# Performance work log

Hardware: AMD Instinct MI355X
Metric: run time of the kernel (lower is better)

Reference implementation:

```python
import jax, jax.numpy as jnp
import numpy as np
from jax import lax

BITWIDTH = 7
EPS = 1e-5


def ti_quant(x):
    """TiFloatToInt8: per-tensor int8 quantization with power-of-2 scale."""
    rng = jnp.max(jnp.abs(x))
    bw = jnp.ceil(jnp.log2(rng))
    exp = bw - BITWIDTH
    q = jnp.clip(jnp.round(x * 2.0 ** (BITWIDTH - bw)), -128.0, 127.0)
    return q, exp


def ti_conv(xv, xe, wv, we, pad):
    """TiConv2d: integer conv (simulated in f32, all values int-valued),
    int32 accumulate, then shift back to 8 bits; exponents add."""
    acc = lax.conv_general_dilated(
        xv, wv, window_strides=(1, 1), padding=[(pad, pad), (pad, pad)],
        dimension_numbers=("NCHW", "OIHW", "NCHW"))
    rng = jnp.max(jnp.abs(acc))
    bw = jnp.ceil(jnp.log2(rng))
    shift = jnp.maximum(bw - BITWIDTH, 0.0)
    q = jnp.clip(jnp.round(acc * 2.0 ** (-shift)), -128.0, 127.0)
    return q, xe + we + shift


def batchnorm(x, gamma, beta):
    # training-mode BN: batch statistics over (N, H, W)
    mean = jnp.mean(x, axis=(0, 2, 3), keepdims=True)
    var = jnp.var(x, axis=(0, 2, 3), keepdims=True)
    g = gamma[None, :, None, None]
    b = beta[None, :, None, None]
    return g * (x - mean) * lax.rsqrt(var + EPS) + b


def setup_inputs() -> dict:
    key = jax.random.key(0)
    k0, k1, k2, k3, k4 = jax.random.split(key, 5)
    B, Cin, Cout, H, W = 32, 128, 256, 56, 56
    x_val = jax.random.randint(k0, (B, Cin, H, W), -128, 128, dtype=jnp.int32)
    x_exp = jnp.zeros((), jnp.float32) - 7.0
    wDW = jnp.round(jnp.clip(jax.random.normal(k1, (Cin, Cin, 3, 3), jnp.float32) * 32.0, -128.0, 127.0))
    wDW_exp = jnp.zeros((), jnp.float32) - 9.0
    wPW = jnp.round(jnp.clip(jax.random.normal(k2, (Cout, Cin, 1, 1), jnp.float32) * 32.0, -128.0, 127.0))
    wPW_exp = jnp.zeros((), jnp.float32) - 9.0
    gamma1 = jnp.ones((Cin,), jnp.float32) + 0.1 * jax.random.normal(k3, (Cin,), jnp.float32)
    beta1 = jnp.zeros((Cin,), jnp.float32)
    gamma2 = jnp.ones((Cout,), jnp.float32) + 0.1 * jax.random.normal(k4, (Cout,), jnp.float32)
    beta2 = jnp.zeros((Cout,), jnp.float32)
    return {"x_val": x_val, "x_exp": x_exp, "wDW": wDW, "wDW_exp": wDW_exp,
            "wPW": wPW, "wPW_exp": wPW_exp, "gamma1": gamma1, "beta1": beta1,
            "gamma2": gamma2, "beta2": beta2}


def reference(x_val, x_exp, wDW, wDW_exp, wPW, wPW_exp, gamma1, beta1, gamma2, beta2):
    xv = x_val.astype(jnp.float32)
    # convDW (3x3, in->in, pad=1)
    q, e = ti_conv(xv, x_exp, wDW, wDW_exp, 1)
    # dequant -> bn1 -> quant
    f = batchnorm(q * 2.0 ** e, gamma1, beta1)
    q, e = ti_quant(f)
    # TiReLU on int values
    q = jnp.maximum(q, 0.0)
    # convPW (1x1, in->out)
    q, e = ti_conv(q, e, wPW, wPW_exp, 0)
    # dequant -> bn2 -> quant -> relu
    f = batchnorm(q * 2.0 ** e, gamma2, beta2)
    q, e = ti_quant(f)
    q = jnp.maximum(q, 0.0)
    return q.astype(jnp.int8), e
```

## Files before the change

### kernel.cpp

```cpp
#include <hip/hip_runtime.h>
#include <cstdint>
#include <cstddef>

#define C1 128
#define C2 256
#define Hh 56
#define Wd 56
#define HW 3136
#define NHW 100352
#define N1 ((size_t)12845056)
#define N2 ((size_t)25690112)
#define XPSZ ((size_t)13778944)
#define NREP 8
#define NB1 392
#define NB2C 392

typedef int v4i __attribute__((ext_vector_type(4)));
typedef int v16i __attribute__((ext_vector_type(16)));

static constexpr size_t OFF_XP = 0;
static constexpr size_t OFF_Q1 = XPSZ;
static constexpr size_t OFF_Q3 = OFF_Q1 + N1;
static constexpr size_t OFF_WQ1 = OFF_Q3 + N2;
static constexpr size_t OFF_WQ2 = OFF_WQ1 + 147456;
static constexpr size_t OFF_STATS = OFF_WQ2 + 32768;

struct Stats {
  int absmax1, absmax2, pad0, pad1;
  float scale1, e1, s2, e2;
  float scaleq2, e3, sf, ef;
  int padA[20];
  int tick1, padB[31];
  int tick2, padC[31];
  int tick3, padD[31];
  int tick4, padE[31];
  int sum1[NREP][C1]; unsigned sumsq1[NREP][C1];
  int min1[NREP][C1], max1[NREP][C1];
  float A1[C1], B1c[C1];
  int sum2[NREP][C2]; unsigned sumsq2[NREP][C2];
  int min2[NREP][C2], max2[NREP][C2];
  float A2[C2], B2c[C2];
};

__global__ __launch_bounds__(256) void k_pre(
    const int* __restrict__ x, signed char* __restrict__ xp,
    const float* __restrict__ wDW, signed char* __restrict__ wq1t,
    const float* __restrict__ wPW, signed char* __restrict__ wq2t,
    Stats* st) {
  __shared__ signed char lds[56 * 132];
  int t = threadIdx.x, bid = blockIdx.x;
  if (bid < 1856) {
    int hh = bid % 58, n = bid / 58;
    int* xpw = (int*)(xp + ((size_t)n * 58 + hh) * 7424);
    if (hh == 0 || hh == 57) {
      for (int o = t; o < 1856; o += 256) xpw[o] = 0;
      return;
    }
    int h = hh - 1;
    const int4* xb4 = (const int4*)(x + (size_t)n * C1 * HW + h * 56);
    for (int idx = t; idx < 1792; idx += 256) {
      int c = idx / 14, wq = idx - c * 14;
      int4 v = xb4[(size_t)c * 784 + wq];
      int w = wq * 4;
      lds[(w + 0) * 132 + c] = (signed char)v.x;
      lds[(w + 1) * 132 + c] = (signed char)v.y;
      lds[(w + 2) * 132 + c] = (signed char)v.z;
      lds[(w + 3) * 132 + c] = (signed char)v.w;
    }
    __syncthreads();
    for (int o = t; o < 1856; o += 256) {
      int kb = o / 232, r = o - kb * 232, ww = r >> 2, cw = r & 3;
      int val = (ww == 0 || ww == 57) ? 0
                : *(const int*)&lds[(ww - 1) * 132 + kb * 16 + cw * 4];
      xpw[o] = val;
    }
    return;
  }
  if (bid < 2432) {
    int idx = (bid - 1856) * 256 + t;
    int co = idx / 1152, r = idx - co * 1152;
    int ci = r / 9, pos = r - ci * 9;
    int k = pos * 128 + ci;
    wq1t[(size_t)(k >> 4) * 2048 + co * 16 + (k & 15)] = (signed char)(int)wDW[idx];
    return;
  }
  if (bid < 2560) {
    int i = (bid - 2432) * 256 + t;
    int co = i >> 7, ci = i & 127;
    wq2t[(size_t)(ci >> 4) * 4096 + co * 16 + (ci & 15)] = (signed char)(int)wPW[i];
    return;
  }
  if (t == 0) {
    st->absmax1 = 0; st->absmax2 = 0;
    st->tick1 = 0; st->tick2 = 0; st->tick3 = 0; st->tick4 = 0;
  }
  for (int c = t; c < NREP * C1; c += 256) {
    ((int*)st->sum1)[c] = 0; ((unsigned*)st->sumsq1)[c] = 0u;
    ((int*)st->min1)[c] = 127; ((int*)st->max1)[c] = -128;
  }
  for (int c = t; c < NREP * C2; c += 256) {
    ((int*)st->sum2)[c] = 0; ((unsigned*)st->sumsq2)[c] = 0u;
    ((int*)st->min2)[c] = 127; ((int*)st->max2)[c] = -128;
  }
}

__device__ inline v4i ld16_lds(const signed char* p) {
  const int2* q = (const int2*)p;
  int2 lo = q[0], hi = q[1];
  v4i r; r[0] = lo.x; r[1] = lo.y; r[2] = hi.x; r[3] = hi.y;
  return r;
}

__device__ inline float bn_affine_v(int sum, unsigned sumsq, int mn, int mx,
                                    float g, float b, float e_in,
                                    float* Aout, float* Bout) {
  double meanq = (double)sum / (double)NHW;
  double varq = (double)sumsq / (double)NHW - meanq * meanq;
  float se = exp2f(e_in);
  float mean = (float)meanq * se;
  float var = (float)varq * se * se;
  float rsq = 1.0f / sqrtf(var + 1e-5f);
  float Avv = g * se * rsq;
  float Bvv = b - g * mean * rsq;
  *Aout = Avv; *Bout = Bvv;
  return fmaxf(fabsf(Avv * (float)mn + Bvv), fabsf(Avv * (float)mx + Bvv));
}

__device__ inline void conv1_mfma(const signed char* __restrict__ xp,
                                  const signed char* __restrict__ wq1t,
                                  int bx, int t, v16i a1[2][4]) {
  int lane = t & 63, wave = t >> 6;
  int half = lane >> 5, l31 = lane & 31;
  size_t g0 = (size_t)bx * 256;

  const signed char* ab[2];
#pragma unroll
  for (int i = 0; i < 2; ++i) {
    size_t gm = g0 + wave * 64 + i * 32 + l31;
    int n = (int)(gm / HW);
    int p = (int)(gm - (size_t)n * HW);
    int h = p / 56, w = p - h * 56;
    ab[i] = xp + ((size_t)n * 58 + h) * 7424 + w * 16 + half * 928;
  }
  const signed char* bb[4];
#pragma unroll
  for (int j = 0; j < 4; ++j)
    bb[j] = wq1t + (size_t)(j * 32 + l31) * 16 + half * 2048;

#pragma unroll
  for (int i = 0; i < 2; ++i)
#pragma unroll
    for (int j = 0; j < 4; ++j)
#pragma unroll
      for (int r = 0; r < 16; ++r) a1[i][j][r] = 0;

#pragma unroll
  for (int pos = 0; pos < 9; ++pos) {
    int kh = pos / 3, kw = pos - kh * 3;
    const signed char* a0p = ab[0] + kh * 7424 + kw * 16;
    const signed char* a1p = ab[1] + kh * 7424 + kw * 16;
#pragma unroll
    for (int kb = 0; kb < 8; kb += 2) {
      v4i af0 = *(const v4i*)(a0p + kb * 928);
      v4i af1 = *(const v4i*)(a1p + kb * 928);
      v4i bf[4];
#pragma unroll
      for (int j = 0; j < 4; ++j)
        bf[j] = *(const v4i*)(bb[j] + pos * 16384 + kb * 2048);
#pragma unroll
      for (int j = 0; j < 4; ++j) {
        a1[0][j] = __builtin_amdgcn_mfma_i32_32x32x32_i8(af0, bf[j], a1[0][j], 0, 0, 0);
        a1[1][j] = __builtin_amdgcn_mfma_i32_32x32x32_i8(af1, bf[j], a1[1][j], 0, 0, 0);
      }
    }
  }
}

__global__ __launch_bounds__(256, 2) void k_conv1f(
    const signed char* __restrict__ xp, const signed char* __restrict__ wq1t,
    signed char* __restrict__ q1, Stats* st,
    const float* __restrict__ x_exp, const float* __restrict__ wDW_exp,
    const float* __restrict__ gamma1, const float* __restrict__ beta1) {
  __shared__ int reda[4];
  __shared__ int vbro;
  __shared__ int qti[256 * 34];
  __shared__ int psum[C1], psq[C1], pmn[C1], pmx[C1];
  __shared__ float redc[2];
  __shared__ int lastf;
  signed char* qt = (signed char*)qti;
  int t = threadIdx.x, lane = t & 63, wave = t >> 6;
  int half = lane >> 5, l31 = lane & 31;
  int rep = blockIdx.x & (NREP - 1);

  v16i a1[2][4];
  conv1_mfma(xp, wq1t, blockIdx.x, t, a1);

  int am = 0;
#pragma unroll
  for (int i = 0; i < 2; ++i)
#pragma unroll
    for (int j = 0; j < 4; ++j)
#pragma unroll
      for (int r = 0; r < 16; ++r) am = max(am, abs(a1[i][j][r]));
  for (int off = 32; off; off >>= 1) am = max(am, __shfl_down(am, off, 64));
  if (lane == 0) reda[wave] = am;
  if (t < C1) { psum[t] = 0; psq[t] = 0; pmn[t] = 127; pmx[t] = -128; }
  __syncthreads();
  if (t == 0)
    atomicMax(&st->absmax1, max(max(reda[0], reda[1]), max(reda[2], reda[3])));
  __syncthreads();

  if (t == 0) {
    atomicAdd(&st->tick1, 1);
    while (atomicAdd(&st->tick1, 0) < NB1)
      __builtin_amdgcn_s_sleep(8);
    vbro = atomicAdd(&st->absmax1, 0);
  }
  __syncthreads();

  int v1 = vbro;
  int pw = 31 - __clz(v1 | 1);
  int bw = ((v1 & (v1 - 1)) == 0) ? pw : pw + 1;
  int sh = max(bw - 7, 0);
  float scale1 = exp2f((float)(-sh));
  float e1 = x_exp[0] + wDW_exp[0] + (float)sh;
  if (blockIdx.x == 0 && t == 0) st->e1 = e1;

#pragma unroll
  for (int j = 0; j < 4; ++j) {
    int sj = 0, sqj = 0, mnj = 127, mxj = -128;
    int c = j * 32 + l31;
#pragma unroll
    for (int i = 0; i < 2; ++i)
#pragma unroll
      for (int reg = 0; reg < 16; ++reg) {
        int av = a1[i][j][reg];
        int row = (reg & 3) + 8 * (reg >> 2) + 4 * half;
        int pix = wave * 64 + i * 32 + row;
        float r = rintf((float)av * scale1);
        r = fminf(fmaxf(r, -128.f), 127.f);
        int qi = (int)r;
        qt[pix * 136 + c] = (signed char)qi;
        sj += qi; sqj += qi * qi; mnj = min(mnj, qi); mxj = max(mxj, qi);
      }
    sj += __shfl_down(sj, 32, 64);
    sqj += __shfl_down(sqj, 32, 64);
    mnj = min(mnj, __shfl_down(mnj, 32, 64));
    mxj = max(mxj, __shfl_down(mxj, 32, 64));
    if (half == 0) {
      atomicAdd(&psum[c], sj); atomicAdd(&psq[c], sqj);
      atomicMin(&pmn[c], mnj); atomicMax(&pmx[c], mxj);
    }
  }
  __syncthreads();
  if (t < C1) {
    atomicAdd(&st->sum1[rep][t], psum[t]);
    atomicAdd(&st->sumsq1[rep][t], (unsigned)psq[t]);
    atomicMin(&st->min1[rep][t], pmn[t]);
    atomicMax(&st->max1[rep][t], pmx[t]);
  }
  int* q1w = (int*)(q1 + (size_t)blockIdx.x * 256 * 128);
  for (int idx = t; idx < 8192; idx += 256)
    q1w[idx] = qti[(idx >> 5) * 34 + (idx & 31)];

  __syncthreads();
  if (t == 0) lastf = (atomicAdd(&st->tick3, 1) == NB1 - 1);
  __syncthreads();
  if (lastf) {
    if (t < C1) {
      int sm = 0; unsigned sq = 0; int mn = 127, mx = -128;
#pragma unroll
      for (int r2 = 0; r2 < NREP; ++r2) {
        sm += atomicAdd(&st->sum1[r2][t], 0);
        sq += atomicAdd(&st->sumsq1[r2][t], 0u);
        mn = min(mn, atomicMin(&st->min1[r2][t], 127));
        mx = max(mx, atomicMax(&st->max1[r2][t], -128));
      }
      float cand = bn_affine_v(sm, sq, mn, mx, gamma1[t], beta1[t], e1,
                               &st->A1[t], &st->B1c[t]);
      for (int off = 32; off; off >>= 1) cand = fmaxf(cand, __shfl_down(cand, off, 64));
      if ((t & 63) == 0) redc[t >> 6] = cand;
    }
    __syncthreads();
    if (t == 0) {
      float rng = fmaxf(redc[0], redc[1]);
      float bwv = ceilf(log2f(rng));
      st->s2 = exp2f(7.0f - bwv);
      st->e2 = bwv - 7.0f;
    }
  }
}

__global__ __launch_bounds__(256, 2) void k_conv2f(
    const signed char* __restrict__ q1, const signed char* __restrict__ wq2t,
    signed char* __restrict__ q3, Stats* st, const float* __restrict__ wPW_exp,
    const float* __restrict__ gamma2, const float* __restrict__ beta2,
    float* __restrict__ out) {
  __shared__ int qti[256 * 34];
  __shared__ int psum[C2], psq[C2], pmn[C2], pmx[C2];
  __shared__ int reda[4];
  __shared__ float red2[4];
  __shared__ int vbro, lastf;
  signed char* qt = (signed char*)qti;

  int t = threadIdx.x, lane = t & 63, wave = t >> 6;
  int half = lane >> 5, l31 = lane & 31;
  size_t g0 = (size_t)blockIdx.x * 256;
  int rep = blockIdx.x & (NREP - 1);

  psum[t] = 0; psq[t] = 0; pmn[t] = 127; pmx[t] = -128;

  int c4 = t & 31;
  float Av[4], Bv[4];
#pragma unroll
  for (int jj = 0; jj < 4; ++jj) {
    Av[jj] = st->A1[c4 * 4 + jj];
    Bv[jj] = st->B1c[c4 * 4 + jj];
  }
  float s2 = st->s2;
  const int* q1w = (const int*)(q1 + g0 * 128);
#pragma unroll
  for (int k = 0; k < 32; ++k) {
    int idx = k * 256 + t;
    int v = q1w[idx];
    int pix = idx >> 5;
    int outv = 0;
#pragma unroll
    for (int jj = 0; jj < 4; ++jj) {
      int b = (signed char)(v >> (8 * jj));
      float y = Av[jj] * (float)b + Bv[jj];
      float r = rintf(y * s2);
      r = fminf(fmaxf(r, -128.f), 127.f);
      r = fmaxf(r, 0.f);
      outv |= ((int)r & 0xff) << (8 * jj);
    }
    qti[pix * 34 + c4] = outv;
  }
  __syncthreads();

  int am2 = 0;
#pragma unroll
  for (int pg = 0; pg < 2; ++pg) {
    int prow = pg * 128 + wave * 32 + l31;
#pragma unroll
    for (int h2 = 0; h2 < 2; ++h2) {
      v16i acc[4];
#pragma unroll
      for (int j = 0; j < 4; ++j)
#pragma unroll
        for (int r = 0; r < 16; ++r) acc[j][r] = 0;
#pragma unroll
      for (int ks = 0; ks < 4; ++ks) {
        v4i af = ld16_lds(&qt[prow * 136 + half * 16 + ks * 32]);
#pragma unroll
        for (int j = 0; j < 4; ++j) {
          v4i bf = *(const v4i*)(wq2t + (size_t)(ks * 2 + half) * 4096 +
                                 ((h2 * 4 + j) * 32 + l31) * 16);
          acc[j] = __builtin_amdgcn_mfma_i32_32x32x32_i8(af, bf, acc[j], 0, 0, 0);
        }
      }
#pragma unroll
      for (int j = 0; j < 4; ++j)
#pragma unroll
        for (int r = 0; r < 16; ++r) am2 = max(am2, abs(acc[j][r]));
    }
  }
  for (int off = 32; off; off >>= 1) am2 = max(am2, __shfl_down(am2, off, 64));
  if (lane == 0) reda[wave] = am2;
  __syncthreads();
  if (t == 0)
    atomicMax(&st->absmax2, max(max(reda[0], reda[1]), max(reda[2], reda[3])));
  __syncthreads();

  if (t == 0) {
    atomicAdd(&st->tick4, 1);
    while (atomicAdd(&st->tick4, 0) < NB2C)
      __builtin_amdgcn_s_sleep(8);
    vbro = atomicAdd(&st->absmax2, 0);
  }
  __syncthreads();

  int v2 = vbro;
  int pw = 31 - __clz(v2 | 1);
  int bw = ((v2 & (v2 - 1)) == 0) ? pw : pw + 1;
  int sh2 = max(bw - 7, 0);
  float scale2 = exp2f((float)(-sh2));
  float e3 = st->e2 + wPW_exp[0] + (float)sh2;
  if (blockIdx.x == 0 && t == 0) st->e3 = e3;

#pragma unroll
  for (int pg = 0; pg < 2; ++pg) {
    int prow = pg * 128 + wave * 32 + l31;
    int* q3w = (int*)(q3 + (size_t)blockIdx.x * 65536 + pg * 32768);
#pragma unroll
    for (int h2 = 0; h2 < 2; ++h2) {
      v16i acc[4];
#pragma unroll
      for (int j = 0; j < 4; ++j)
#pragma unroll
        for (int r = 0; r < 16; ++r) acc[j][r] = 0;
#pragma unroll
      for (int ks = 0; ks < 4; ++ks) {
        v4i af = ld16_lds(&qt[prow * 136 + half * 16 + ks * 32]);
#pragma unroll
        for (int j = 0; j < 4; ++j) {
          v4i bf = *(const v4i*)(wq2t + (size_t)(ks * 2 + half) * 4096 +
                                 ((h2 * 4 + j) * 32 + l31) * 16);
          acc[j] = __builtin_amdgcn_mfma_i32_32x32x32_i8(af, bf, acc[j], 0, 0, 0);
        }
      }
#pragma unroll
      for (int j = 0; j < 4; ++j) {
        int jg = h2 * 4 + j;
        int c = jg * 32 + l31;
        int sj = 0, sqj = 0, mnj = 127, mxj = -128;
#pragma unroll
        for (int rg = 0; rg < 4; ++rg) {
          int pk = 0;
#pragma unroll
          for (int b = 0; b < 4; ++b) {
            float r = rintf((float)acc[j][4 * rg + b] * scale2);
            r = fminf(fmaxf(r, -128.f), 127.f);
            int qi = (int)r;
            pk |= (qi & 0xff) << (8 * b);
            sj += qi; sqj += qi * qi; mnj = min(mnj, qi); mxj = max(mxj, qi);
          }
          q3w[((wave * 8 + jg) * 4 + rg) * 64 + lane] = pk;
        }
        sj += __shfl_down(sj, 32, 64);
        sqj += __shfl_down(sqj, 32, 64);
        mnj = min(mnj, __shfl_down(mnj, 32, 64));
        mxj = max(mxj, __shfl_down(mxj, 32, 64));
        if (half == 0) {
          atomicAdd(&psum[c], sj); atomicAdd(&psq[c], sqj);
          atomicMin(&pmn[c], mnj); atomicMax(&pmx[c], mxj);
        }
      }
    }
  }
  __syncthreads();
  atomicAdd(&st->sum2[rep][t], psum[t]);
  atomicAdd(&st->sumsq2[rep][t], (unsigned)psq[t]);
  atomicMin(&st->min2[rep][t], pmn[t]);
  atomicMax(&st->max2[rep][t], pmx[t]);

  __syncthreads();
  if (t == 0) lastf = (atomicAdd(&st->tick2, 1) == NB2C - 1);
  __syncthreads();
  if (lastf) {
    int sm = 0; unsigned sq = 0; int mn = 127, mx = -128;
#pragma unroll
    for (int r2 = 0; r2 < NREP; ++r2) {
      sm += atomicAdd(&st->sum2[r2][t], 0);
      sq += atomicAdd(&st->sumsq2[r2][t], 0u);
      mn = min(mn, atomicMin(&st->min2[r2][t], 127));
      mx = max(mx, atomicMax(&st->max2[r2][t], -128));
    }
    float cand = bn_affine_v(sm, sq, mn, mx, gamma2[t], beta2[t], e3,
                             &st->A2[t], &st->B2c[t]);
    for (int off = 32; off; off >>= 1) cand = fmaxf(cand, __shfl_down(cand, off, 64));
    if (lane == 0) red2[wave] = cand;
    __syncthreads();
    if (t == 0) {
      float rng = fmaxf(fmaxf(red2[0], red2[1]), fmaxf(red2[2], red2[3]));
      float bwv = ceilf(log2f(rng));
      st->sf = exp2f(7.0f - bwv);
      st->ef = bwv - 7.0f;
      out[N2] = bwv - 7.0f;
    }
  }
}

__global__ __launch_bounds__(256) void k_out(
    const signed char* __restrict__ q3, const Stats* __restrict__ st,
    float* __restrict__ out) {
  __shared__ int ldsc[256 * 17];
  int t = threadIdx.x, lane = t & 63, wave = t >> 6;
  int bid = blockIdx.x;
  size_t g0 = (size_t)bid * 64;
  int n = (int)(g0 / HW), p0 = (int)(g0 - (size_t)n * HW);
  const int* q3r = (const int*)(q3 + (size_t)(bid >> 1) * 32768) + (bid & 1) * 4096;
#pragma unroll
  for (int k = 0; k < 16; ++k) {
    int i = k * 256 + t;
    int ln = i & 63, rg = (i >> 6) & 3, j = (i >> 8) & 7, wv = (i >> 11) & 1;
    int v = q3r[i];
    int c = j * 32 + (ln & 31);
    int psub = wv * 8 + 2 * rg + (ln >> 5);
    ldsc[c * 17 + psub] = v;
  }
  __syncthreads();
  float sf = st->sf;
  float* ob = out + (size_t)n * C2 * HW + p0 + lane;
#pragma unroll
  for (int cg = 0; cg < 64; ++cg) {
    int c = wave * 64 + ((cg + wave * 16) & 63);
    int vv = ldsc[c * 17 + (lane >> 2)];
    float y = st->A2[c] * (float)((signed char)(vv >> (8 * (lane & 3)))) + st->B2c[c];
    float r = rintf(y * sf);
    r = fminf(fmaxf(r, -128.f), 127.f);
    ob[(size_t)c * HW] = fmaxf(r, 0.f);
  }
}

extern "C" void kernel_launch(void* const* d_in, const int* in_sizes, int n_in,
                              void* d_out, int out_size, void* d_ws, size_t ws_size,
                              hipStream_t stream) {
  const int* x = (const int*)d_in[0];
  const float* x_exp = (const float*)d_in[1];
  const float* wDW = (const float*)d_in[2];
  const float* wDW_exp = (const float*)d_in[3];
  const float* wPW = (const float*)d_in[4];
  const float* wPW_exp = (const float*)d_in[5];
  const float* gamma1 = (const float*)d_in[6];
  const float* beta1 = (const float*)d_in[7];
  const float* gamma2 = (const float*)d_in[8];
  const float* beta2 = (const float*)d_in[9];
  float* out = (float*)d_out;

  char* ws = (char*)d_ws;
  signed char* xp2 = (signed char*)(ws + OFF_XP);
  signed char* q1 = (signed char*)(ws + OFF_Q1);
  signed char* q3 = (signed char*)(ws + OFF_Q3);
  signed char* wq1t = (signed char*)(ws + OFF_WQ1);
  signed char* wq2t = (signed char*)(ws + OFF_WQ2);
  Stats* st = (Stats*)(ws + OFF_STATS);

  hipLaunchKernelGGL(k_pre, dim3(2561), dim3(256), 0, stream,
                     x, xp2, wDW, wq1t, wPW, wq2t, st);
  hipLaunchKernelGGL(k_conv1f, dim3(NB1), dim3(256), 0, stream,
                     xp2, wq1t, q1, st, x_exp, wDW_exp, gamma1, beta1);
  hipLaunchKernelGGL(k_conv2f, dim3(NB2C), dim3(256), 0, stream,
                     q1, wq2t, q3, st, wPW_exp, gamma2, beta2, out);
  hipLaunchKernelGGL(k_out, dim3(1568), dim3(256), 0, stream, q3, st, out);
}
```

Measured before the change: 261.4 us.

## Fuse output BN/quant stage into conv2 kernel via grid-wide barrier

Removes the separate k_out launch and folds the final BN2 affine, quantize and ReLU pass into k_conv2f. After the last block computes the BN2 parameters, it publishes them as replicated copies via atomics and bumps a new tick. Every block spins on that tick, then rewrites four 64-pixel output tiles from q3. This saves a kernel launch and the stats reload, but adds a second grid-wide spin barrier and relies on all 392 blocks being co-resident. Spreading the replicas is meant to avoid atomic hotspots.

```diff
diff --git a/kernel.cpp b/kernel.cpp
--- a/kernel.cpp
+++ b/kernel.cpp
@@ -34,12 +34,14 @@
   int tick2, padC[31];
   int tick3, padD[31];
   int tick4, padE[31];
+  int tick5, padF[31];
   int sum1[NREP][C1]; unsigned sumsq1[NREP][C1];
   int min1[NREP][C1], max1[NREP][C1];
   float A1[C1], B1c[C1];
   int sum2[NREP][C2]; unsigned sumsq2[NREP][C2];
   int min2[NREP][C2], max2[NREP][C2];
-  float A2[C2], B2c[C2];
+  float A2rep[NREP][C2], B2rep[NREP][C2];
+  float sfrep[NREP * 32];
 };
 
 __global__ __launch_bounds__(256) void k_pre(
@@ -92,7 +94,7 @@
   }
   if (t == 0) {
     st->absmax1 = 0; st->absmax2 = 0;
-    st->tick1 = 0; st->tick2 = 0; st->tick3 = 0; st->tick4 = 0;
+    st->tick1 = 0; st->tick2 = 0; st->tick3 = 0; st->tick4 = 0; st->tick5 = 0;
   }
   for (int c = t; c < NREP * C1; c += 256) {
     ((int*)st->sum1)[c] = 0; ((unsigned*)st->sumsq1)[c] = 0u;
@@ -101,7 +103,9 @@
   for (int c = t; c < NREP * C2; c += 256) {
     ((int*)st->sum2)[c] = 0; ((unsigned*)st->sumsq2)[c] = 0u;
     ((int*)st->min2)[c] = 127; ((int*)st->max2)[c] = -128;
-  }
+    ((float*)st->A2rep)[c] = 0.f; ((float*)st->B2rep)[c] = 0.f;
+  }
+  if (t < NREP * 32) st->sfrep[t] = 0.f;
 }
 
 __device__ inline v4i ld16_lds(const signed char* p) {
@@ -300,6 +304,7 @@
   __shared__ int psum[C2], psq[C2], pmn[C2], pmx[C2];
   __shared__ int reda[4];
   __shared__ float red2[4];
+  __shared__ float A2l[C2], B2l[C2], sfl[1];
   __shared__ int vbro, lastf;
   signed char* qt = (signed char*)qti;
 
@@ -386,7 +391,6 @@
   int sh2 = max(bw - 7, 0);
   float scale2 = exp2f((float)(-sh2));
   float e3 = st->e2 + wPW_exp[0] + (float)sh2;
-  if (blockIdx.x == 0 && t == 0) st->e3 = e3;
 
 #pragma unroll
   for (int pg = 0; pg < 2; ++pg) {
@@ -456,50 +460,69 @@
       mn = min(mn, atomicMin(&st->min2[r2][t], 127));
       mx = max(mx, atomicMax(&st->max2[r2][t], -128));
     }
-    float cand = bn_affine_v(sm, sq, mn, mx, gamma2[t], beta2[t], e3,
-                             &st->A2[t], &st->B2c[t]);
+    float Avv, Bvv;
+    float cand = bn_affine_v(sm, sq, mn, mx, gamma2[t], beta2[t], e3, &Avv, &Bvv);
+#pragma unroll
+    for (int r2 = 0; r2 < NREP; ++r2) {
+      atomicAdd(&st->A2rep[r2][t], Avv);
+      atomicAdd(&st->B2rep[r2][t], Bvv);
+    }
     for (int off = 32; off; off >>= 1) cand = fmaxf(cand, __shfl_down(cand, off, 64));
     if (lane == 0) red2[wave] = cand;
     __syncthreads();
     if (t == 0) {
       float rng = fmaxf(fmaxf(red2[0], red2[1]), fmaxf(red2[2], red2[3]));
       float bwv = ceilf(log2f(rng));
-      st->sf = exp2f(7.0f - bwv);
+      float sfv = exp2f(7.0f - bwv);
       st->ef = bwv - 7.0f;
       out[N2] = bwv - 7.0f;
-    }
-  }
-}
-
-__global__ __launch_bounds__(256) void k_out(
-    const signed char* __restrict__ q3, const Stats* __restrict__ st,
-    float* __restrict__ out) {
-  __shared__ int ldsc[256 * 17];
-  int t = threadIdx.x, lane = t & 63, wave = t >> 6;
-  int bid = blockIdx.x;
-  size_t g0 = (size_t)bid * 64;
-  int n = (int)(g0 / HW), p0 = (int)(g0 - (size_t)n * HW);
-  const int* q3r = (const int*)(q3 + (size_t)(bid >> 1) * 32768) + (bid & 1) * 4096;
-#pragma unroll
-  for (int k = 0; k < 16; ++k) {
-    int i = k * 256 + t;
-    int ln = i & 63, rg = (i >> 6) & 3, j = (i >> 8) & 7, wv = (i >> 11) & 1;
-    int v = q3r[i];
-    int c = j * 32 + (ln & 31);
-    int psub = wv * 8 + 2 * rg + (ln >> 5);
-    ldsc[c * 17 + psub] = v;
-  }
-  __syncthreads();
-  float sf = st->sf;
-  float* ob = out + (size_t)n * C2 * HW + p0 + lane;
-#pragma unroll
-  for (int cg = 0; cg < 64; ++cg) {
-    int c = wave * 64 + ((cg + wave * 16) & 63);
-    int vv = ldsc[c * 17 + (lane >> 2)];
-    float y = st->A2[c] * (float)((signed char)(vv >> (8 * (lane & 3)))) + st->B2c[c];
-    float r = rintf(y * sf);
-    r = fminf(fmaxf(r, -128.f), 127.f);
-    ob[(size_t)c * HW] = fmaxf(r, 0.f);
+#pragma unroll
+      for (int r2 = 0; r2 < NREP; ++r2)
+        atomicAdd(&st->sfrep[r2 * 32], sfv);
+    }
+    __syncthreads();
+    if (t == 0) atomicAdd(&st->tick5, 1);
+  }
+
+  if (t == 0) {
+    while (atomicAdd(&st->tick5, 0) < 1)
+      __builtin_amdgcn_s_sleep(8);
+    sfl[0] = atomicAdd(&st->sfrep[rep * 32], 0.f);
+  }
+  __syncthreads();
+  A2l[t] = atomicAdd(&st->A2rep[rep][t], 0.f);
+  B2l[t] = atomicAdd(&st->B2rep[rep][t], 0.f);
+  __syncthreads();
+  float sf = sfl[0];
+
+  int* ldsc = qti;
+#pragma unroll
+  for (int sub = 0; sub < 4; ++sub) {
+    int bo = (int)blockIdx.x * 4 + sub;
+    size_t go = (size_t)bo * 64;
+    int n2 = (int)(go / HW), p0 = (int)(go - (size_t)n2 * HW);
+    const int* q3r = (const int*)(q3 + (size_t)(bo >> 1) * 32768) + (bo & 1) * 4096;
+    __syncthreads();
+#pragma unroll
+    for (int k = 0; k < 16; ++k) {
+      int i = k * 256 + t;
+      int ln = i & 63, rg = (i >> 6) & 3, j = (i >> 8) & 7, wv = (i >> 11) & 1;
+      int v = q3r[i];
+      int c = j * 32 + (ln & 31);
+      int psub = wv * 8 + 2 * rg + (ln >> 5);
+      ldsc[c * 17 + psub] = v;
+    }
+    __syncthreads();
+    float* ob = out + (size_t)n2 * C2 * HW + p0 + lane;
+#pragma unroll
+    for (int cg = 0; cg < 64; ++cg) {
+      int c = wave * 64 + ((cg + wave * 16) & 63);
+      int vv = ldsc[c * 17 + (lane >> 2)];
+      float y = A2l[c] * (float)((signed char)(vv >> (8 * (lane & 3)))) + B2l[c];
+      float r = rintf(y * sf);
+      r = fminf(fmaxf(r, -128.f), 127.f);
+      ob[(size_t)c * HW] = fmaxf(r, 0.f);
+    }
   }
 }
 
@@ -532,5 +555,4 @@
                      xp2, wq1t, q1, st, x_exp, wDW_exp, gamma1, beta1);
   hipLaunchKernelGGL(k_conv2f, dim3(NB2C), dim3(256), 0, stream,
                      q1, wq2t, q3, st, wPW_exp, gamma2, beta2, out);
-  hipLaunchKernelGGL(k_out, dim3(1568), dim3(256), 0, stream, q3, st, out);
-}
+}
```

Result: slower. 284.7 us (+8.9%).
